# Optimization experiments

Hardware: AMD Instinct MI355X
Metric: run time of the kernel (lower is better)

Reference implementation:

```python
import jax, jax.numpy as jnp
import numpy as np

BITS = 4
MAXQ = (1 << BITS) - 1          # 15
ELEMS = 32 // BITS              # values packed per int32
GROUPSIZE = 128
M, K, N = 4096, 4096, 11008
G = K // GROUPSIZE              # 32 groups


def dequantize(qweight, scales, qzeros, g_idx):
    """Unpack GPTQ int4 weights -> fp16 [K, N], matching matmul_248_kernel."""
    K_ = g_idx.shape[0]
    N_ = scales.shape[1]
    k = jnp.arange(K_)
    # weight: value k,n packed in qweight[k // ELEMS, n] at bit offset (k % ELEMS)*BITS
    w = (qweight[k // ELEMS] >> ((k % ELEMS) * BITS)[:, None].astype(jnp.int32)) & MAXQ  # [K, N]
    # zeros: value g,n packed in qzeros[g, n // ELEMS] at bit offset (n % ELEMS)*BITS; kernel adds +1
    n = jnp.arange(N_)
    z = ((qzeros[:, n // ELEMS] >> ((n % ELEMS) * BITS)[None, :].astype(jnp.int32)) & MAXQ) + 1  # [G, N]
    gi = g_idx.astype(jnp.int32)
    # b = (b - zeros) * scales, per-group via g_idx row mapping
    W = scales[gi] * (w - z[gi]).astype(scales.dtype)  # fp16 [K, N]
    return W


def setup_inputs() -> dict:
    key = jax.random.key(0)
    k1, k2, k3, k4 = jax.random.split(key, 4)
    x = (jax.random.normal(k1, (M, K), dtype=jnp.float32) * 0.05).astype(jnp.float16)
    imin = jnp.iinfo(jnp.int32).min
    imax = jnp.iinfo(jnp.int32).max
    qweight = jax.random.randint(k2, (K // ELEMS, N), imin, imax, dtype=jnp.int32)
    qzeros = jax.random.randint(k3, (G, N // ELEMS), imin, imax, dtype=jnp.int32)
    scales = (jax.random.uniform(k4, (G, N), dtype=jnp.float32) * 0.009 + 0.001).astype(jnp.float16)
    g_idx = (jnp.arange(K, dtype=jnp.int32) // GROUPSIZE).astype(jnp.int32)
    return {"x": x, "qweight": qweight, "scales": scales, "qzeros": qzeros, "g_idx": g_idx}


def reference(x, qweight, scales, qzeros, g_idx):
    W = dequantize(qweight, scales, qzeros, g_idx)
    # fp16 inputs, fp32 accumulation, fp16 store (as in the Triton kernel)
    out = jnp.dot(x, W, preferred_element_type=jnp.float32).astype(jnp.float16)
    return out
```

## Files before the change

kernel.cpp:

```cpp
#include <hip/hip_runtime.h>

typedef unsigned short u16;
typedef unsigned int   u32;
typedef _Float16       f16;

#define M_DIM 4096
#define K_DIM 4096
#define N_DIM 11008
#define NQ8   (N_DIM / 8)
#define BM 128
#define BN 128
#define BK 32
#define BKP 40

typedef f16   f16x8 __attribute__((ext_vector_type(8)));
typedef f16   f16x2 __attribute__((ext_vector_type(2)));
typedef float f32x4 __attribute__((ext_vector_type(4)));

typedef __attribute__((address_space(1))) void GV;
typedef __attribute__((address_space(3))) void LV;

__device__ __forceinline__ u32 pk2(float lo, float hi) {
    return __builtin_bit_cast(u32, __builtin_amdgcn_cvt_pkrtz(lo, hi));
}

__global__ __launch_bounds__(256) void cvt_x(const float* __restrict__ x, f16* __restrict__ xh) {
    const size_t t = (size_t)blockIdx.x * 256 + threadIdx.x;
    const float4* p = (const float4*)(x + t * 8);
    float4 a0 = p[0], a1 = p[1];
    uint4 v;
    v.x = pk2(a0.x, a1.x); v.y = pk2(a0.y, a1.y);
    v.z = pk2(a0.z, a1.z); v.w = pk2(a0.w, a1.w);
    *(uint4*)(xh + t * 8) = v;
}

template<bool PRE>
__global__ __launch_bounds__(256, 2)
void gptq_gemm(const float* __restrict__ x, const f16* __restrict__ xh,
               const int* __restrict__ qw, const float* __restrict__ sc,
               const int* __restrict__ qz, float* __restrict__ out)
{
    constexpr int AK = PRE ? 32 : 40;
    __shared__ __align__(16) f16 As[BM * AK];
    __shared__ __align__(16) f16 Bs[BN * BKP];

    const int tid  = threadIdx.x;
    const int lane = tid & 63;
    const int wave = tid >> 6;
    const int quad = lane >> 4;
    const int l15  = lane & 15;
    const int wm   = (wave & 1) * 64;
    const int wn   = (wave >> 1) * 64;

    const int m0 = blockIdx.y * BM;
    const int n0 = blockIdx.x * BN;

    const f16* agh0 = xh + (size_t)(m0 + (tid >> 2)) * K_DIM + (tid & 3) * 8;
    const f16* agh1 = agh0 + (size_t)64 * K_DIM;
    f16* al0 = As + tid * 8;
    f16* al1 = As + 2048 + tid * 8;
    const float* agf = x + (size_t)(m0 + (tid >> 1)) * K_DIM + (tid & 1) * 16;
    f16* alf = As + (tid >> 1) * AK + (tid & 1) * 16;

    const int dn  = tid & 127;
    const int dkq = tid >> 7;
    const int gn  = n0 + dn;
    const int zsh = (gn & 7) * 4;
    const int*   qwp = qw + gn;
    const int*   qzp = qz + (gn >> 3);
    const float* scp = sc + gn;
    f16* bs0 = Bs + dn * BKP + dkq * 8;

    f32x4 acc[4][4];
    #pragma unroll
    for (int i = 0; i < 4; i++)
        #pragma unroll
        for (int j = 0; j < 4; j++)
            acc[i][j] = (f32x4){0.f, 0.f, 0.f, 0.f};

    for (int g = 0; g < K_DIM / 128; g++) {
        const u32 zq = (u32)qzp[(size_t)g * NQ8];
        const int z1 = (int)((zq >> zsh) & 15u) + 1;
        const float s = scp[(size_t)g * N_DIM];
        const f16 sh = (f16)s;
        const f16 bh = (f16)(-(float)(1024 + z1));
        const f16x2 s2 = {sh, sh};
        const f16x2 b2 = {bh, bh};

        #pragma unroll
        for (int t = 0; t < 4; t++) {
            const int kt = g * 4 + t;

            if constexpr (PRE) {
                __builtin_amdgcn_global_load_lds((GV*)(agh0 + kt * BK), (LV*)al0, 16, 0, 0);
                __builtin_amdgcn_global_load_lds((GV*)(agh1 + kt * BK), (LV*)al1, 16, 0, 0);
            }

            uint4 bv[2];
            #pragma unroll
            for (int i = 0; i < 2; i++) {
                const u32 q = (u32)qwp[(size_t)(4 * kt + dkq + 2 * i) * N_DIM];
                u32 pk[4];
                #pragma unroll
                for (int j = 0; j < 4; j++) {
                    const u32 mbits = ((q >> (4 * j)) & 0x000F000Fu) | 0x64006400u;
                    f16x2 v2 = __builtin_bit_cast(f16x2, mbits);
                    f16x2 w2 = (v2 + b2) * s2;
                    pk[j] = __builtin_bit_cast(u32, w2);
                }
                bv[i].x = pk[0]; bv[i].y = pk[1]; bv[i].z = pk[2]; bv[i].w = pk[3];
            }

            if constexpr (!PRE) {
                const float4* agp = (const float4*)(agf + kt * BK);
                float4 a0 = agp[0], a1 = agp[1], a2 = agp[2], a3 = agp[3];
                uint4 av0, av1;
                av0.x = pk2(a0.x, a1.x); av0.y = pk2(a0.y, a1.y);
                av0.z = pk2(a0.z, a1.z); av0.w = pk2(a0.w, a1.w);
                av1.x = pk2(a2.x, a3.x); av1.y = pk2(a2.y, a3.y);
                av1.z = pk2(a2.z, a3.z); av1.w = pk2(a2.w, a3.w);
                *(uint4*)(alf)     = av0;
                *(uint4*)(alf + 8) = av1;
            }
            *(uint4*)(bs0)      = bv[0];
            *(uint4*)(bs0 + 16) = bv[1];
            __syncthreads();

            f16x8 af[4], bfr[4];
            #pragma unroll
            for (int t2 = 0; t2 < 4; t2++) {
                af[t2]  = *(const f16x8*)(As + (wm + t2 * 16 + l15) * AK  + quad * 8);
                bfr[t2] = *(const f16x8*)(Bs + (wn + t2 * 16 + l15) * BKP + quad * 8);
            }
            #pragma unroll
            for (int i = 0; i < 4; i++)
                #pragma unroll
                for (int j = 0; j < 4; j++)
                    acc[i][j] = __builtin_amdgcn_mfma_f32_16x16x32_f16(af[i], bfr[j], acc[i][j], 0, 0, 0);
            __syncthreads();
        }
    }

    #pragma unroll
    for (int i = 0; i < 4; i++) {
        const int mrow = m0 + wm + i * 16 + quad * 4;
        #pragma unroll
        for (int j = 0; j < 4; j++) {
            const int ncol = n0 + wn + j * 16 + l15;
            float* op = out + (size_t)mrow * N_DIM + ncol;
            #pragma unroll
            for (int r = 0; r < 4; r++)
                op[(size_t)r * N_DIM] = acc[i][j][r];
        }
    }
}

extern "C" void kernel_launch(void* const* d_in, const int* in_sizes, int n_in,
                              void* d_out, int out_size, void* d_ws, size_t ws_size,
                              hipStream_t stream) {
    const float* x  = (const float*)d_in[0];
    const int*   qw = (const int*)d_in[1];
    const float* sc = (const float*)d_in[2];
    const int*   qz = (const int*)d_in[3];
    float* out = (float*)d_out;
    f16*   xh  = (f16*)d_ws;

    dim3 grid(N_DIM / BN, M_DIM / BM);
    const bool pre = ws_size >= (size_t)M_DIM * K_DIM * sizeof(f16);
    if (pre) {
        cvt_x<<<(M_DIM * K_DIM / 8) / 256, 256, 0, stream>>>(x, xh);
        gptq_gemm<true><<<grid, 256, 0, stream>>>(x, xh, qw, sc, qz, out);
    } else {
        gptq_gemm<false><<<grid, 256, 0, stream>>>(x, xh, qw, sc, qz, out);
    }
}
```

Before: 638.3 us.

## Rewrite pre-converted path as 256x256 double-buffered pipelined GEMM with swizzled LDS

```diff
diff --git a/kernel.cpp b/kernel.cpp
--- a/kernel.cpp
+++ b/kernel.cpp
@@ -8,10 +8,6 @@
 #define K_DIM 4096
 #define N_DIM 11008
 #define NQ8   (N_DIM / 8)
-#define BM 128
-#define BN 128
-#define BK 32
-#define BKP 40
 
 typedef f16   f16x8 __attribute__((ext_vector_type(8)));
 typedef f16   f16x2 __attribute__((ext_vector_type(2)));
@@ -19,6 +15,9 @@
 
 typedef __attribute__((address_space(1))) void GV;
 typedef __attribute__((address_space(3))) void LV;
+
+#define SFENCE() __builtin_amdgcn_sched_barrier(0)
+#define BAR()    __builtin_amdgcn_s_barrier()
 
 __device__ __forceinline__ u32 pk2(float lo, float hi) {
     return __builtin_bit_cast(u32, __builtin_amdgcn_cvt_pkrtz(lo, hi));
@@ -34,15 +33,248 @@
     *(uint4*)(xh + t * 8) = v;
 }
 
-template<bool PRE>
+__device__ __forceinline__ uint4 dq8(u32 q, f16x2 b2, f16x2 s2) {
+    u32 pk[4];
+    #pragma unroll
+    for (int j = 0; j < 4; j++) {
+        const u32 mb = ((q >> (4 * j)) & 0x000F000Fu) | 0x64006400u;
+        f16x2 v2 = __builtin_bit_cast(f16x2, mb);
+        f16x2 w2 = (v2 + b2) * s2;
+        pk[j] = __builtin_bit_cast(u32, w2);
+    }
+    uint4 r; r.x = pk[0]; r.y = pk[1]; r.z = pk[2]; r.w = pk[3];
+    return r;
+}
+
+#define BM 256
+#define BN 256
+#define BK 64
+#define NKT (K_DIM / BK)
+
+template<int AI, int CJ>
+__device__ __forceinline__ void mfma_block(f32x4 (&acc)[8][4], const f16x8 (&af)[4][2],
+                                           const f16x8 (&bf)[2][2]) {
+    #pragma unroll
+    for (int mf = 0; mf < 4; ++mf)
+        #pragma unroll
+        for (int nf = 0; nf < 2; ++nf)
+            #pragma unroll
+            for (int ks = 0; ks < 2; ++ks)
+                acc[AI + mf][CJ + nf] = __builtin_amdgcn_mfma_f32_16x16x32_f16(
+                    af[mf][ks], bf[nf][ks], acc[AI + mf][CJ + nf], 0, 0, 0);
+}
+
+#define MFMA_PHASE(AI, BF, CJ)                \
+    BAR();                                    \
+    __builtin_amdgcn_s_setprio(1);            \
+    mfma_block<AI, CJ>(acc, af, BF);          \
+    __builtin_amdgcn_s_setprio(0);            \
+    BAR();
+
+__global__ __launch_bounds__(512, 2)
+void gptq_gemm_big(const f16* __restrict__ xh, const int* __restrict__ qw,
+                   const float* __restrict__ sc, const int* __restrict__ qz,
+                   float* __restrict__ out)
+{
+    __shared__ __align__(16) f16 As[2][BM * BK];
+    __shared__ __align__(16) f16 Bs[2][BN * BK];
+
+    const int tid  = threadIdx.x;
+    const int lane = tid & 63;
+    const int wave = tid >> 6;
+    const int quad = lane >> 4;
+    const int l15  = lane & 15;
+    const int sw   = l15 & 7;
+    const int wm   = (wave >> 2) * 128;
+    const int wn   = (wave & 3) * 64;
+
+    const int bid0 = blockIdx.y * 43 + blockIdx.x;
+    const int bid  = (bid0 & 7) * 86 + (bid0 >> 3);
+    const int n0 = (bid % 43) * BN;
+    const int m0 = (bid / 43) * BM;
+
+    const int cko[2] = { (quad ^ sw) * 8, ((4 + quad) ^ sw) * 8 };
+
+    const int arow = tid >> 3;
+    const int acnk = (tid & 7) ^ (arow & 7);
+    const f16* ag[4];
+    #pragma unroll
+    for (int j = 0; j < 4; ++j)
+        ag[j] = xh + (size_t)(m0 + j * 64 + arow) * K_DIM + acnk * 8;
+
+    const int bn   = tid >> 1;
+    const int bsub = tid & 1;
+    const int gn   = n0 + bn;
+    const int zsh  = (gn & 7) * 4;
+    const int* qwp[4];
+    #pragma unroll
+    for (int i = 0; i < 4; ++i)
+        qwp[i] = qw + (size_t)(bsub * 4 + i) * N_DIM + gn;
+    const int*   qzp = qz + (gn >> 3);
+    const float* scp = sc + gn;
+    int bwo[4];
+    #pragma unroll
+    for (int i = 0; i < 4; ++i)
+        bwo[i] = (bn * 8 + ((bsub * 4 + i) ^ (bn & 7))) * 8;
+
+    f32x4 acc[8][4];
+    #pragma unroll
+    for (int i = 0; i < 8; ++i)
+        #pragma unroll
+        for (int j = 0; j < 4; ++j)
+            acc[i][j] = (f32x4){0.f, 0.f, 0.f, 0.f};
+
+    u32 bq_c[4]; u32 zq_c; float sv_c;
+
+    {
+        const u32 zq0  = (u32)qzp[0];
+        const float sv0 = scp[0];
+        u32 bq0[4];
+        #pragma unroll
+        for (int i = 0; i < 4; ++i) bq0[i] = (u32)qwp[i][0];
+        SFENCE();
+        #pragma unroll
+        for (int j = 0; j < 4; ++j)
+            __builtin_amdgcn_global_load_lds((GV*)ag[j], (LV*)(&As[0][0] + (tid + j * 512) * 8), 16, 0, 0);
+        SFENCE();
+        #pragma unroll
+        for (int i = 0; i < 4; ++i) bq_c[i] = (u32)qwp[i][(size_t)8 * N_DIM];
+        zq_c = (u32)qzp[0];
+        sv_c = scp[0];
+        const int z1 = (int)((zq0 >> zsh) & 15u) + 1;
+        const f16 sh = (f16)sv0;
+        const f16 bh = (f16)(-(float)(1024 + z1));
+        const f16x2 s2 = {sh, sh}, b2 = {bh, bh};
+        #pragma unroll
+        for (int i = 0; i < 4; ++i)
+            *(uint4*)(&Bs[0][0] + bwo[i]) = dq8(bq0[i], b2, s2);
+        SFENCE();
+        asm volatile("s_waitcnt vmcnt(6)" ::: "memory");
+        asm volatile("s_waitcnt lgkmcnt(0)" ::: "memory");
+        BAR();
+    }
+
+    #pragma unroll 1
+    for (int t = 0; t < NKT - 1; ++t) {
+        const int b = t & 1;
+        const f16* Ab = &As[b][0];
+        const f16* Bb = &Bs[b][0];
+        f16* Ad = &As[b ^ 1][0];
+        f16* Bd = &Bs[b ^ 1][0];
+
+        const int z1 = (int)((zq_c >> zsh) & 15u) + 1;
+        const f16 sh = (f16)sv_c;
+        const f16 bh = (f16)(-(float)(1024 + z1));
+        const f16x2 s2 = {sh, sh}, b2 = {bh, bh};
+
+        f16x8 af[4][2], bf0[2][2], bf1[2][2];
+
+        #pragma unroll
+        for (int mf = 0; mf < 4; ++mf)
+            #pragma unroll
+            for (int ks = 0; ks < 2; ++ks)
+                af[mf][ks] = *(const f16x8*)(Ab + (wm + mf * 16 + l15) * 64 + cko[ks]);
+        #pragma unroll
+        for (int nf = 0; nf < 2; ++nf)
+            #pragma unroll
+            for (int ks = 0; ks < 2; ++ks)
+                bf0[nf][ks] = *(const f16x8*)(Bb + (wn + nf * 16 + l15) * 64 + cko[ks]);
+        SFENCE();
+        __builtin_amdgcn_global_load_lds((GV*)(ag[0] + (t + 1) * BK), (LV*)(Ad + tid * 8), 16, 0, 0);
+        __builtin_amdgcn_global_load_lds((GV*)(ag[1] + (t + 1) * BK), (LV*)(Ad + (tid + 512) * 8), 16, 0, 0);
+        SFENCE();
+        *(uint4*)(Bd + bwo[0]) = dq8(bq_c[0], b2, s2);
+        *(uint4*)(Bd + bwo[1]) = dq8(bq_c[1], b2, s2);
+        MFMA_PHASE(0, bf0, 0)
+
+        #pragma unroll
+        for (int nf = 0; nf < 2; ++nf)
+            #pragma unroll
+            for (int ks = 0; ks < 2; ++ks)
+                bf1[nf][ks] = *(const f16x8*)(Bb + (wn + 32 + nf * 16 + l15) * 64 + cko[ks]);
+        SFENCE();
+        __builtin_amdgcn_global_load_lds((GV*)(ag[2] + (t + 1) * BK), (LV*)(Ad + (tid + 1024) * 8), 16, 0, 0);
+        __builtin_amdgcn_global_load_lds((GV*)(ag[3] + (t + 1) * BK), (LV*)(Ad + (tid + 1536) * 8), 16, 0, 0);
+        SFENCE();
+        *(uint4*)(Bd + bwo[2]) = dq8(bq_c[2], b2, s2);
+        *(uint4*)(Bd + bwo[3]) = dq8(bq_c[3], b2, s2);
+        MFMA_PHASE(0, bf1, 2)
+
+        #pragma unroll
+        for (int mf = 0; mf < 4; ++mf)
+            #pragma unroll
+            for (int ks = 0; ks < 2; ++ks)
+                af[mf][ks] = *(const f16x8*)(Ab + (wm + 64 + mf * 16 + l15) * 64 + cko[ks]);
+        {
+            const int t2 = (t + 2 < NKT) ? (t + 2) : (NKT - 1);
+            #pragma unroll
+            for (int i = 0; i < 4; ++i)
+                bq_c[i] = (u32)qwp[i][(size_t)(t2 * 8) * N_DIM];
+            zq_c = (u32)qzp[(size_t)(t2 >> 1) * NQ8];
+            sv_c = scp[(size_t)(t2 >> 1) * N_DIM];
+        }
+        MFMA_PHASE(4, bf1, 2)
+
+        SFENCE();
+        asm volatile("s_waitcnt vmcnt(6)" ::: "memory");
+        asm volatile("s_waitcnt lgkmcnt(0)" ::: "memory");
+        MFMA_PHASE(4, bf0, 0)
+    }
+
+    {
+        const f16* Ab = &As[1][0];
+        const f16* Bb = &Bs[1][0];
+        f16x8 af[4][2], bf0[2][2], bf1[2][2];
+        #pragma unroll
+        for (int nf = 0; nf < 2; ++nf)
+            #pragma unroll
+            for (int ks = 0; ks < 2; ++ks) {
+                bf0[nf][ks] = *(const f16x8*)(Bb + (wn + nf * 16 + l15) * 64 + cko[ks]);
+                bf1[nf][ks] = *(const f16x8*)(Bb + (wn + 32 + nf * 16 + l15) * 64 + cko[ks]);
+            }
+        #pragma unroll
+        for (int mh = 0; mh < 2; ++mh) {
+            #pragma unroll
+            for (int mf = 0; mf < 4; ++mf)
+                #pragma unroll
+                for (int ks = 0; ks < 2; ++ks)
+                    af[mf][ks] = *(const f16x8*)(Ab + (wm + mh * 64 + mf * 16 + l15) * 64 + cko[ks]);
+            #pragma unroll
+            for (int mf = 0; mf < 4; ++mf)
+                #pragma unroll
+                for (int nf = 0; nf < 2; ++nf)
+                    #pragma unroll
+                    for (int ks = 0; ks < 2; ++ks) {
+                        acc[mh * 4 + mf][nf]     = __builtin_amdgcn_mfma_f32_16x16x32_f16(
+                            af[mf][ks], bf0[nf][ks], acc[mh * 4 + mf][nf], 0, 0, 0);
+                        acc[mh * 4 + mf][2 + nf] = __builtin_amdgcn_mfma_f32_16x16x32_f16(
+                            af[mf][ks], bf1[nf][ks], acc[mh * 4 + mf][2 + nf], 0, 0, 0);
+                    }
+        }
+    }
+
+    #pragma unroll
+    for (int i = 0; i < 8; ++i) {
+        const int mrow = m0 + wm + i * 16 + quad * 4;
+        #pragma unroll
+        for (int j = 0; j < 4; ++j) {
+            const int ncol = n0 + wn + j * 16 + l15;
+            float* op = out + (size_t)mrow * N_DIM + ncol;
+            #pragma unroll
+            for (int r = 0; r < 4; ++r)
+                op[(size_t)r * N_DIM] = acc[i][j][r];
+        }
+    }
+}
+
 __global__ __launch_bounds__(256, 2)
-void gptq_gemm(const float* __restrict__ x, const f16* __restrict__ xh,
-               const int* __restrict__ qw, const float* __restrict__ sc,
-               const int* __restrict__ qz, float* __restrict__ out)
+void gptq_gemm_f32(const float* __restrict__ x, const int* __restrict__ qw,
+                   const float* __restrict__ sc, const int* __restrict__ qz,
+                   float* __restrict__ out)
 {
-    constexpr int AK = PRE ? 32 : 40;
-    __shared__ __align__(16) f16 As[BM * AK];
-    __shared__ __align__(16) f16 Bs[BN * BKP];
+    constexpr int AK = 40;
+    __shared__ __align__(16) f16 As[128 * AK];
+    __shared__ __align__(16) f16 Bs[128 * 40];
 
     const int tid  = threadIdx.x;
     const int lane = tid & 63;
@@ -51,14 +283,9 @@
     const int l15  = lane & 15;
     const int wm   = (wave & 1) * 64;
     const int wn   = (wave >> 1) * 64;
-
-    const int m0 = blockIdx.y * BM;
-    const int n0 = blockIdx.x * BN;
-
-    const f16* agh0 = xh + (size_t)(m0 + (tid >> 2)) * K_DIM + (tid & 3) * 8;
-    const f16* agh1 = agh0 + (size_t)64 * K_DIM;
-    f16* al0 = As + tid * 8;
-    f16* al1 = As + 2048 + tid * 8;
+    const int m0 = blockIdx.y * 128;
+    const int n0 = blockIdx.x * 128;
+
     const float* agf = x + (size_t)(m0 + (tid >> 1)) * K_DIM + (tid & 1) * 16;
     f16* alf = As + (tid >> 1) * AK + (tid & 1) * 16;
 
@@ -69,7 +296,7 @@
     const int*   qwp = qw + gn;
     const int*   qzp = qz + (gn >> 3);
     const float* scp = sc + gn;
-    f16* bs0 = Bs + dn * BKP + dkq * 8;
+    f16* bs0 = Bs + dn * 40 + dkq * 8;
 
     f32x4 acc[4][4];
     #pragma unroll
@@ -84,44 +311,25 @@
         const float s = scp[(size_t)g * N_DIM];
         const f16 sh = (f16)s;
         const f16 bh = (f16)(-(float)(1024 + z1));
-        const f16x2 s2 = {sh, sh};
-        const f16x2 b2 = {bh, bh};
+        const f16x2 s2 = {sh, sh}, b2 = {bh, bh};
 
         #pragma unroll
         for (int t = 0; t < 4; t++) {
             const int kt = g * 4 + t;
-
-            if constexpr (PRE) {
-                __builtin_amdgcn_global_load_lds((GV*)(agh0 + kt * BK), (LV*)al0, 16, 0, 0);
-                __builtin_amdgcn_global_load_lds((GV*)(agh1 + kt * BK), (LV*)al1, 16, 0, 0);
-            }
-
             uint4 bv[2];
             #pragma unroll
-            for (int i = 0; i < 2; i++) {
-                const u32 q = (u32)qwp[(size_t)(4 * kt + dkq + 2 * i) * N_DIM];
-                u32 pk[4];
-                #pragma unroll
-                for (int j = 0; j < 4; j++) {
-                    const u32 mbits = ((q >> (4 * j)) & 0x000F000Fu) | 0x64006400u;
-                    f16x2 v2 = __builtin_bit_cast(f16x2, mbits);
-                    f16x2 w2 = (v2 + b2) * s2;
-                    pk[j] = __builtin_bit_cast(u32, w2);
-                }
-                bv[i].x = pk[0]; bv[i].y = pk[1]; bv[i].z = pk[2]; bv[i].w = pk[3];
-            }
-
-            if constexpr (!PRE) {
-                const float4* agp = (const float4*)(agf + kt * BK);
-                float4 a0 = agp[0], a1 = agp[1], a2 = agp[2], a3 = agp[3];
-                uint4 av0, av1;
-                av0.x = pk2(a0.x, a1.x); av0.y = pk2(a0.y, a1.y);
-                av0.z = pk2(a0.z, a1.z); av0.w = pk2(a0.w, a1.w);
-                av1.x = pk2(a2.x, a3.x); av1.y = pk2(a2.y, a3.y);
-                av1.z = pk2(a2.z, a3.z); av1.w = pk2(a2.w, a3.w);
-                *(uint4*)(alf)     = av0;
-                *(uint4*)(alf + 8) = av1;
-            }
+            for (int i = 0; i < 2; i++)
+                bv[i] = dq8((u32)qwp[(size_t)(4 * kt + dkq + 2 * i) * N_DIM], b2, s2);
+
+            const float4* agp = (const float4*)(agf + kt * 32);
+            float4 a0 = agp[0], a1 = agp[1], a2 = agp[2], a3 = agp[3];
+            uint4 av0, av1;
+            av0.x = pk2(a0.x, a1.x); av0.y = pk2(a0.y, a1.y);
+            av0.z = pk2(a0.z, a1.z); av0.w = pk2(a0.w, a1.w);
+            av1.x = pk2(a2.x, a3.x); av1.y = pk2(a2.y, a3.y);
+            av1.z = pk2(a2.z, a3.z); av1.w = pk2(a2.w, a3.w);
+            *(uint4*)(alf)     = av0;
+            *(uint4*)(alf + 8) = av1;
             *(uint4*)(bs0)      = bv[0];
             *(uint4*)(bs0 + 16) = bv[1];
             __syncthreads();
@@ -129,8 +337,8 @@
             f16x8 af[4], bfr[4];
             #pragma unroll
             for (int t2 = 0; t2 < 4; t2++) {
-                af[t2]  = *(const f16x8*)(As + (wm + t2 * 16 + l15) * AK  + quad * 8);
-                bfr[t2] = *(const f16x8*)(Bs + (wn + t2 * 16 + l15) * BKP + quad * 8);
+                af[t2]  = *(const f16x8*)(As + (wm + t2 * 16 + l15) * AK + quad * 8);
+                bfr[t2] = *(const f16x8*)(Bs + (wn + t2 * 16 + l15) * 40 + quad * 8);
             }
             #pragma unroll
             for (int i = 0; i < 4; i++)
@@ -165,12 +373,11 @@
     float* out = (float*)d_out;
     f16*   xh  = (f16*)d_ws;
 
-    dim3 grid(N_DIM / BN, M_DIM / BM);
     const bool pre = ws_size >= (size_t)M_DIM * K_DIM * sizeof(f16);
     if (pre) {
         cvt_x<<<(M_DIM * K_DIM / 8) / 256, 256, 0, stream>>>(x, xh);
-        gptq_gemm<true><<<grid, 256, 0, stream>>>(x, xh, qw, sc, qz, out);
+        gptq_gemm_big<<<dim3(N_DIM / BN, M_DIM / BM), 512, 0, stream>>>(xh, qw, sc, qz, out);
     } else {
-        gptq_gemm<false><<<grid, 256, 0, stream>>>(x, xh, qw, sc, qz, out);
-    }
-}
+        gptq_gemm_f32<<<dim3(N_DIM / 128, M_DIM / 128), 256, 0, stream>>>(x, qw, sc, qz, out);
+    }
+}
```

Result: slower. 701.9 us (+10.0%).

## Add 256x256 double-buffered GPTQ GEMM kernel with swizzled LDS and interleaved staging

Applied to the files above, without the earlier changes.

```diff
diff --git a/kernel.cpp b/kernel.cpp
--- a/kernel.cpp
+++ b/kernel.cpp
@@ -8,17 +8,22 @@
 #define K_DIM 4096
 #define N_DIM 11008
 #define NQ8   (N_DIM / 8)
-#define BM 128
-#define BN 128
-#define BK 32
-#define BKP 40
 
 typedef f16   f16x8 __attribute__((ext_vector_type(8)));
 typedef f16   f16x2 __attribute__((ext_vector_type(2)));
 typedef float f32x4 __attribute__((ext_vector_type(4)));
+typedef u32   u32x4 __attribute__((ext_vector_type(4)));
+typedef float f32x4v __attribute__((ext_vector_type(4)));
 
 typedef __attribute__((address_space(1))) void GV;
 typedef __attribute__((address_space(3))) void LV;
+typedef __attribute__((address_space(3))) f16   lf16;
+typedef __attribute__((address_space(3))) f16x8 lf16x8;
+typedef __attribute__((address_space(3))) u32x4 lu32x4;
+
+#define BAR()    __builtin_amdgcn_s_barrier()
+#define WAITV(N) asm volatile("s_waitcnt vmcnt(" #N ")" ::: "memory")
+#define WAITL0() asm volatile("s_waitcnt lgkmcnt(0)" ::: "memory")
 
 __device__ __forceinline__ u32 pk2(float lo, float hi) {
     return __builtin_bit_cast(u32, __builtin_amdgcn_cvt_pkrtz(lo, hi));
@@ -28,21 +33,229 @@
     const size_t t = (size_t)blockIdx.x * 256 + threadIdx.x;
     const float4* p = (const float4*)(x + t * 8);
     float4 a0 = p[0], a1 = p[1];
-    uint4 v;
+    u32x4 v;
     v.x = pk2(a0.x, a1.x); v.y = pk2(a0.y, a1.y);
     v.z = pk2(a0.z, a1.z); v.w = pk2(a0.w, a1.w);
-    *(uint4*)(xh + t * 8) = v;
-}
-
-template<bool PRE>
+    *(u32x4*)(xh + t * 8) = v;
+}
+
+__device__ __forceinline__ u32x4 dq8(u32 q, f16x2 b2, f16x2 s2) {
+    u32 pk[4];
+    #pragma unroll
+    for (int j = 0; j < 4; j++) {
+        const u32 mb = ((q >> (4 * j)) & 0x000F000Fu) | 0x64006400u;
+        f16x2 v2 = __builtin_bit_cast(f16x2, mb);
+        f16x2 w2 = (v2 + b2) * s2;
+        pk[j] = __builtin_bit_cast(u32, w2);
+    }
+    u32x4 r; r.x = pk[0]; r.y = pk[1]; r.z = pk[2]; r.w = pk[3];
+    return r;
+}
+
+#define BM 256
+#define BN 256
+#define BK 64
+
+#define LDA(MH, BUF) do { \
+    _Pragma("unroll") for (int mf = 0; mf < 4; ++mf) { \
+        af[mf][0] = *(const lf16x8*)(pAr0 + (BUF)*16384 + (MH)*4096 + mf*1024); \
+        af[mf][1] = *(const lf16x8*)(pAr1 + (BUF)*16384 + (MH)*4096 + mf*1024); \
+    } } while (0)
+
+#define LDB(BF, NH, BUF) do { \
+    _Pragma("unroll") for (int nf = 0; nf < 2; ++nf) { \
+        BF[nf][0] = *(const lf16x8*)(pBr0 + (BUF)*16384 + (NH)*2048 + nf*1024); \
+        BF[nf][1] = *(const lf16x8*)(pBr1 + (BUF)*16384 + (NH)*2048 + nf*1024); \
+    } } while (0)
+
+#define STAGE_A(J, BUF, PTR) __builtin_amdgcn_global_load_lds( \
+    (GV*)(PTR), (LV*)(&As[0][0] + (BUF)*16384 + (tid + (J)*512)*8), 16, 0, 0)
+
+#define STAGE_B(R, BUF, BQ, B2, S2) \
+    *(lu32x4*)(pBw + (BUF)*16384 + bwo[R]) = dq8((BQ)[R], (B2), (S2))
+
+#define MFMA16(AI, BF, CJ) do { \
+    _Pragma("unroll") for (int ks = 0; ks < 2; ++ks) \
+    _Pragma("unroll") for (int mf = 0; mf < 4; ++mf) \
+    _Pragma("unroll") for (int nf = 0; nf < 2; ++nf) \
+        acc[(AI)+mf][(CJ)+nf] = __builtin_amdgcn_mfma_f32_16x16x32_f16( \
+            af[mf][ks], (BF)[nf][ks], acc[(AI)+mf][(CJ)+nf], 0, 0, 0); \
+    } while (0)
+
+#define PRIO1() __builtin_amdgcn_s_setprio(1)
+#define PRIO0() __builtin_amdgcn_s_setprio(0)
+
+__global__ __launch_bounds__(512, 2)
+void gptq_gemm_big(const f16* __restrict__ xh, const int* __restrict__ qw,
+                   const float* __restrict__ sc, const int* __restrict__ qz,
+                   float* __restrict__ out)
+{
+    __shared__ __align__(16) f16 As[2][BM * BK];
+    __shared__ __align__(16) f16 Bs[2][BN * BK];
+
+    const int tid  = threadIdx.x;
+    const int lane = tid & 63;
+    const int wave = tid >> 6;
+    const int quad = lane >> 4;
+    const int l15  = lane & 15;
+    const int sw   = l15 & 7;
+    const int wm   = (wave >> 2) * 128;
+    const int wn   = (wave & 3) * 64;
+
+    const int bid0 = blockIdx.y * 43 + blockIdx.x;
+    const int bid  = (bid0 & 7) * 86 + (bid0 >> 3);
+    const int n0 = (bid % 43) * BN;
+    const int m0 = (bid / 43) * BM;
+
+    const int cko0 = (quad ^ sw) * 8;
+    const int cko1 = ((4 + quad) ^ sw) * 8;
+
+    const lf16* pAr0 = (const lf16*)&As[0][0] + (wm + l15) * 64 + cko0;
+    const lf16* pAr1 = (const lf16*)&As[0][0] + (wm + l15) * 64 + cko1;
+    const lf16* pBr0 = (const lf16*)&Bs[0][0] + (wn + l15) * 64 + cko0;
+    const lf16* pBr1 = (const lf16*)&Bs[0][0] + (wn + l15) * 64 + cko1;
+    lf16* pBw = (lf16*)&Bs[0][0];
+
+    const int arow = tid >> 3;
+    const int acnk = (tid & 7) ^ (arow & 7);
+    const f16* agp[4];
+    #pragma unroll
+    for (int j = 0; j < 4; ++j)
+        agp[j] = xh + (size_t)(m0 + j * 64 + arow) * K_DIM + acnk * 8;
+
+    const int bn   = tid >> 1;
+    const int bsub = tid & 1;
+    const int qr0  = bsub * 4;
+    const int gn   = n0 + bn;
+    const int zsh  = (gn & 7) * 4;
+    const int*   qcol = qw + gn;
+    const int*   qzp  = qz + (gn >> 3);
+    const float* scp  = sc + gn;
+    int bwo[4];
+    #pragma unroll
+    for (int i = 0; i < 4; ++i)
+        bwo[i] = (bn * 8 + ((qr0 + i) ^ (bn & 7))) * 8;
+
+    f32x4 acc[8][4];
+    #pragma unroll
+    for (int i = 0; i < 8; ++i)
+        #pragma unroll
+        for (int j = 0; j < 4; ++j)
+            acc[i][j] = (f32x4){0.f, 0.f, 0.f, 0.f};
+
+    f16x8 af[4][2], bf0[2][2], bf1[2][2];
+    u32 bqA[4], bqB[4];
+    u32 zq_c; float sv_c;
+    u32 zq_n; float sv_n;
+
+    {
+        zq_c = (u32)qzp[0];
+        sv_c = scp[0];
+        u32 bq0[4];
+        #pragma unroll
+        for (int j = 0; j < 4; ++j) bq0[j] = (u32)qcol[(size_t)(qr0 + j) * N_DIM];
+        #pragma unroll
+        for (int j = 0; j < 4; ++j) STAGE_A(j, 0, agp[j]);
+        #pragma unroll
+        for (int j = 0; j < 4; ++j) bqA[j] = (u32)qcol[(size_t)(8 + qr0 + j) * N_DIM];
+        const f16 sh = (f16)sv_c;
+        const f16 bh = (f16)(-(float)(1025 + (int)((zq_c >> zsh) & 15u)));
+        const f16x2 s2 = {sh, sh}, b2 = {bh, bh};
+        #pragma unroll
+        for (int r = 0; r < 4; ++r) STAGE_B(r, 0, bq0, b2, s2);
+        WAITV(0); WAITL0();
+        BAR();
+    }
+
+    #pragma unroll 1
+    for (int i = 0; i < 32; ++i) {
+        const f16 shc = (f16)sv_c;
+        const f16 bhc = (f16)(-(float)(1025 + (int)((zq_c >> zsh) & 15u)));
+        const f16x2 s2c = {shc, shc}, b2c = {bhc, bhc};
+        const int t2 = (i < 31) ? 2 * i + 2 : 63;
+        const int t3 = (i < 31) ? 2 * i + 3 : 63;
+        const int gnx = (i < 31) ? i + 1 : 31;
+        const int a5off = (i < 31) ? 128 : 64;
+
+        LDA(0, 0);
+        LDB(bf0, 0, 0);
+        STAGE_A(0, 1, agp[0] + 64);
+        STAGE_A(2, 1, agp[2] + 64);
+        #pragma unroll
+        for (int j = 0; j < 4; ++j) bqB[j] = (u32)qcol[(size_t)(t2 * 8 + qr0 + j) * N_DIM];
+        zq_n = (u32)qzp[(size_t)gnx * NQ8];
+        sv_n = scp[(size_t)gnx * N_DIM];
+        STAGE_B(0, 1, bqA, b2c, s2c);
+        BAR(); PRIO1(); MFMA16(0, bf0, 0); PRIO0(); BAR();
+
+        LDB(bf1, 1, 0);
+        STAGE_A(1, 1, agp[1] + 64);
+        STAGE_A(3, 1, agp[3] + 64);
+        STAGE_B(1, 1, bqA, b2c, s2c);
+        BAR(); PRIO1(); MFMA16(0, bf1, 2); PRIO0(); WAITV(10); BAR();
+
+        LDA(1, 0);
+        STAGE_B(2, 1, bqA, b2c, s2c);
+        BAR(); PRIO1(); MFMA16(4, bf1, 2); PRIO0(); BAR();
+
+        STAGE_B(3, 1, bqA, b2c, s2c);
+        BAR(); PRIO1(); MFMA16(4, bf0, 0); PRIO0(); WAITV(2); WAITL0(); BAR();
+
+        const f16 shn = (f16)sv_n;
+        const f16 bhn = (f16)(-(float)(1025 + (int)((zq_n >> zsh) & 15u)));
+        const f16x2 s2n = {shn, shn}, b2n = {bhn, bhn};
+
+        LDA(0, 1);
+        LDB(bf0, 0, 1);
+        STAGE_A(0, 0, agp[0] + a5off);
+        STAGE_A(2, 0, agp[2] + a5off);
+        #pragma unroll
+        for (int j = 0; j < 4; ++j) bqA[j] = (u32)qcol[(size_t)(t3 * 8 + qr0 + j) * N_DIM];
+        STAGE_B(0, 0, bqB, b2n, s2n);
+        BAR(); PRIO1(); MFMA16(0, bf0, 0); PRIO0(); BAR();
+
+        LDB(bf1, 1, 1);
+        STAGE_A(1, 0, agp[1] + a5off);
+        STAGE_A(3, 0, agp[3] + a5off);
+        STAGE_B(1, 0, bqB, b2n, s2n);
+        BAR(); PRIO1(); MFMA16(0, bf1, 2); PRIO0(); WAITV(8); BAR();
+
+        LDA(1, 1);
+        STAGE_B(2, 0, bqB, b2n, s2n);
+        BAR(); PRIO1(); MFMA16(4, bf1, 2); PRIO0(); BAR();
+
+        STAGE_B(3, 0, bqB, b2n, s2n);
+        BAR(); PRIO1(); MFMA16(4, bf0, 0); PRIO0(); WAITV(2); WAITL0(); BAR();
+
+        zq_c = zq_n; sv_c = sv_n;
+        #pragma unroll
+        for (int j = 0; j < 4; ++j) agp[j] += 128;
+    }
+
+    WAITV(0); WAITL0();
+
+    #pragma unroll
+    for (int i = 0; i < 8; ++i) {
+        const int mrow = m0 + wm + i * 16 + quad * 4;
+        #pragma unroll
+        for (int j = 0; j < 4; ++j) {
+            const int ncol = n0 + wn + j * 16 + l15;
+            float* op = out + (size_t)mrow * N_DIM + ncol;
+            #pragma unroll
+            for (int r = 0; r < 4; ++r)
+                op[(size_t)r * N_DIM] = acc[i][j][r];
+        }
+    }
+}
+
 __global__ __launch_bounds__(256, 2)
-void gptq_gemm(const float* __restrict__ x, const f16* __restrict__ xh,
-               const int* __restrict__ qw, const float* __restrict__ sc,
-               const int* __restrict__ qz, float* __restrict__ out)
+void gptq_gemm_f32(const float* __restrict__ x, const int* __restrict__ qw,
+                   const float* __restrict__ sc, const int* __restrict__ qz,
+                   float* __restrict__ out)
 {
-    constexpr int AK = PRE ? 32 : 40;
-    __shared__ __align__(16) f16 As[BM * AK];
-    __shared__ __align__(16) f16 Bs[BN * BKP];
+    constexpr int AK = 40;
+    __shared__ __align__(16) f16 As[128 * AK];
+    __shared__ __align__(16) f16 Bs[128 * 40];
 
     const int tid  = threadIdx.x;
     const int lane = tid & 63;
@@ -51,14 +264,9 @@
     const int l15  = lane & 15;
     const int wm   = (wave & 1) * 64;
     const int wn   = (wave >> 1) * 64;
-
-    const int m0 = blockIdx.y * BM;
-    const int n0 = blockIdx.x * BN;
-
-    const f16* agh0 = xh + (size_t)(m0 + (tid >> 2)) * K_DIM + (tid & 3) * 8;
-    const f16* agh1 = agh0 + (size_t)64 * K_DIM;
-    f16* al0 = As + tid * 8;
-    f16* al1 = As + 2048 + tid * 8;
+    const int m0 = blockIdx.y * 128;
+    const int n0 = blockIdx.x * 128;
+
     const float* agf = x + (size_t)(m0 + (tid >> 1)) * K_DIM + (tid & 1) * 16;
     f16* alf = As + (tid >> 1) * AK + (tid & 1) * 16;
 
@@ -69,7 +277,7 @@
     const int*   qwp = qw + gn;
     const int*   qzp = qz + (gn >> 3);
     const float* scp = sc + gn;
-    f16* bs0 = Bs + dn * BKP + dkq * 8;
+    f16* bs0 = Bs + dn * 40 + dkq * 8;
 
     f32x4 acc[4][4];
     #pragma unroll
@@ -84,53 +292,34 @@
         const float s = scp[(size_t)g * N_DIM];
         const f16 sh = (f16)s;
         const f16 bh = (f16)(-(float)(1024 + z1));
-        const f16x2 s2 = {sh, sh};
-        const f16x2 b2 = {bh, bh};
+        const f16x2 s2 = {sh, sh}, b2 = {bh, bh};
 
         #pragma unroll
         for (int t = 0; t < 4; t++) {
             const int kt = g * 4 + t;
-
-            if constexpr (PRE) {
-                __builtin_amdgcn_global_load_lds((GV*)(agh0 + kt * BK), (LV*)al0, 16, 0, 0);
-                __builtin_amdgcn_global_load_lds((GV*)(agh1 + kt * BK), (LV*)al1, 16, 0, 0);
-            }
-
-            uint4 bv[2];
-            #pragma unroll
-            for (int i = 0; i < 2; i++) {
-                const u32 q = (u32)qwp[(size_t)(4 * kt + dkq + 2 * i) * N_DIM];
-                u32 pk[4];
-                #pragma unroll
-                for (int j = 0; j < 4; j++) {
-                    const u32 mbits = ((q >> (4 * j)) & 0x000F000Fu) | 0x64006400u;
-                    f16x2 v2 = __builtin_bit_cast(f16x2, mbits);
-                    f16x2 w2 = (v2 + b2) * s2;
-                    pk[j] = __builtin_bit_cast(u32, w2);
-                }
-                bv[i].x = pk[0]; bv[i].y = pk[1]; bv[i].z = pk[2]; bv[i].w = pk[3];
-            }
-
-            if constexpr (!PRE) {
-                const float4* agp = (const float4*)(agf + kt * BK);
-                float4 a0 = agp[0], a1 = agp[1], a2 = agp[2], a3 = agp[3];
-                uint4 av0, av1;
-                av0.x = pk2(a0.x, a1.x); av0.y = pk2(a0.y, a1.y);
-                av0.z = pk2(a0.z, a1.z); av0.w = pk2(a0.w, a1.w);
-                av1.x = pk2(a2.x, a3.x); av1.y = pk2(a2.y, a3.y);
-                av1.z = pk2(a2.z, a3.z); av1.w = pk2(a2.w, a3.w);
-                *(uint4*)(alf)     = av0;
-                *(uint4*)(alf + 8) = av1;
-            }
-            *(uint4*)(bs0)      = bv[0];
-            *(uint4*)(bs0 + 16) = bv[1];
+            u32x4 bv[2];
+            #pragma unroll
+            for (int i = 0; i < 2; i++)
+                bv[i] = dq8((u32)qwp[(size_t)(4 * kt + dkq + 2 * i) * N_DIM], b2, s2);
+
+            const float4* agp2 = (const float4*)(agf + kt * 32);
+            float4 a0 = agp2[0], a1 = agp2[1], a2 = agp2[2], a3 = agp2[3];
+            u32x4 av0, av1;
+            av0.x = pk2(a0.x, a1.x); av0.y = pk2(a0.y, a1.y);
+            av0.z = pk2(a0.z, a1.z); av0.w = pk2(a0.w, a1.w);
+            av1.x = pk2(a2.x, a3.x); av1.y = pk2(a2.y, a3.y);
+            av1.z = pk2(a2.z, a3.z); av1.w = pk2(a2.w, a3.w);
+            *(u32x4*)(alf)     = av0;
+            *(u32x4*)(alf + 8) = av1;
+            *(u32x4*)(bs0)      = bv[0];
+            *(u32x4*)(bs0 + 16) = bv[1];
             __syncthreads();
 
             f16x8 af[4], bfr[4];
             #pragma unroll
             for (int t2 = 0; t2 < 4; t2++) {
-                af[t2]  = *(const f16x8*)(As + (wm + t2 * 16 + l15) * AK  + quad * 8);
-                bfr[t2] = *(const f16x8*)(Bs + (wn + t2 * 16 + l15) * BKP + quad * 8);
+                af[t2]  = *(const f16x8*)(As + (wm + t2 * 16 + l15) * AK + quad * 8);
+                bfr[t2] = *(const f16x8*)(Bs + (wn + t2 * 16 + l15) * 40 + quad * 8);
             }
             #pragma unroll
             for (int i = 0; i < 4; i++)
@@ -165,12 +354,11 @@
     float* out = (float*)d_out;
     f16*   xh  = (f16*)d_ws;
 
-    dim3 grid(N_DIM / BN, M_DIM / BM);
     const bool pre = ws_size >= (size_t)M_DIM * K_DIM * sizeof(f16);
     if (pre) {
         cvt_x<<<(M_DIM * K_DIM / 8) / 256, 256, 0, stream>>>(x, xh);
-        gptq_gemm<true><<<grid, 256, 0, stream>>>(x, xh, qw, sc, qz, out);
+        gptq_gemm_big<<<dim3(N_DIM / BN, M_DIM / BM), 512, 0, stream>>>(xh, qw, sc, qz, out);
     } else {
-        gptq_gemm<false><<<grid, 256, 0, stream>>>(x, xh, qw, sc, qz, out);
-    }
-}
+        gptq_gemm_f32<<<dim3(N_DIM / 128, M_DIM / 128), 256, 0, stream>>>(x, qw, sc, qz, out);
+    }
+}
```

After: 602.5 us. -5.6%, faster.
